# Optimization experiments

Measured on AMD Instinct MI355X. Metric: run time of the kernel, lower is better.

## Reference

```python
import jax, jax.numpy as jnp
import numpy as np

EPS = 1e-5
NEG_SLOPE = 0.2
GN_GROUPS = 8


def conv2d(x, w, b):
    # x: [B,C,H,W], w: [O,I,3,3]
    y = jax.lax.conv_general_dilated(
        x, w, window_strides=(1, 1), padding=((1, 1), (1, 1)),
        dimension_numbers=('NCHW', 'OIHW', 'NCHW'))
    return y + b[None, :, None, None]


def conv3d_d(x, w, b):
    # x: [B,C,D,H,W], w: [O,I,3,1,1] -> conv along D only
    y = jax.lax.conv_general_dilated(
        x, w, window_strides=(1, 1, 1), padding=((1, 1), (0, 0), (0, 0)),
        dimension_numbers=('NCDHW', 'OIDHW', 'NCDHW'))
    return y + b[None, :, None, None, None]


def group_norm(x, gamma, beta):
    # x: [B,C,D,H,W]; normalize per group over (C/g, D, H, W)
    B, C, D, H, W = x.shape
    xg = x.reshape(B, GN_GROUPS, C // GN_GROUPS, D, H, W)
    mu = jnp.mean(xg, axis=(2, 3, 4, 5), keepdims=True)
    var = jnp.var(xg, axis=(2, 3, 4, 5), keepdims=True)
    xn = ((xg - mu) * jax.lax.rsqrt(var + EPS)).reshape(B, C, D, H, W)
    return xn * gamma[None, :, None, None, None] + beta[None, :, None, None, None]


def setup_inputs() -> dict:
    key = jax.random.key(0)
    ks = jax.random.split(key, 8)
    C = 32
    B, D, H, W = 2, 24, 160, 160
    s = lambda fan: 1.0 / np.sqrt(fan)
    return {
        'x': jax.random.normal(ks[0], (B, C, D, H, W), jnp.float32),
        'w_f1': jax.random.normal(ks[1], (2 * C, C, 3, 1, 1), jnp.float32) * s(C * 3),
        'b_f1': jnp.zeros((2 * C,), jnp.float32),
        'gn_g': jnp.ones((2 * C,), jnp.float32),
        'gn_b': jnp.zeros((2 * C,), jnp.float32),
        'w_f2': jax.random.normal(ks[2], (C, 2 * C, 3, 1, 1), jnp.float32) * s(2 * C * 3),
        'b_f2': jnp.zeros((C,), jnp.float32),
        'w_u': jax.random.normal(ks[3], (C, 2 * C, 3, 3), jnp.float32) * s(2 * C * 9),
        'b_u': jnp.zeros((C,), jnp.float32),
        'w_r': jax.random.normal(ks[4], (C, 2 * C, 3, 3), jnp.float32) * s(2 * C * 9),
        'b_r': jnp.zeros((C,), jnp.float32),
        'w_o': jax.random.normal(ks[5], (C, 2 * C, 3, 3), jnp.float32) * s(2 * C * 9),
        'b_o': jnp.zeros((C,), jnp.float32),
    }


def reference(x, w_f1, b_f1, gn_g, gn_b, w_f2, b_f2, w_u, b_u, w_r, b_r, w_o, b_o):
    B, C, D, H, W = x.shape

    # slice_flow: Conv3d(C->2C,(3,1,1)) -> GroupNorm(8) -> LeakyReLU(0.2) -> Conv3d(2C->C,(3,1,1))
    sf = conv3d_d(x, w_f1, b_f1)
    sf = group_norm(sf, gn_g, gn_b)
    sf = jnp.where(sf >= 0, sf, NEG_SLOPE * sf)
    slice_features = conv3d_d(sf, w_f2, b_f2)

    def gru_step(h, xd):
        combined = jnp.concatenate([xd, h], axis=1)
        update = jax.nn.sigmoid(conv2d(combined, w_u, b_u))
        reset = jax.nn.sigmoid(conv2d(combined, w_r, b_r))
        combined_reset = jnp.concatenate([xd, reset * h], axis=1)
        cand = jnp.tanh(conv2d(combined_reset, w_o, b_o))
        h_new = (1.0 - update) * h + update * cand
        return h_new, h_new

    xd = jnp.moveaxis(x, 2, 0)  # [D,B,C,H,W]
    h0 = jnp.zeros((B, C, H, W), x.dtype)
    _, fwd = jax.lax.scan(gru_step, h0, xd)                 # [D,B,C,H,W]
    _, bwd = jax.lax.scan(gru_step, h0, xd, reverse=True)   # aligned with xd order

    enhanced = xd + fwd + bwd                                # [D,B,C,H,W]
    return jnp.moveaxis(enhanced, 0, 2) + slice_features
```

## Files before the change

### kernel.cpp

```cpp
#include <hip/hip_runtime.h>
#include <hip/hip_bf16.h>
#include <stdint.h>

#define EPS_GN 1e-5f
#define NEG_SLOPE 0.2f

static constexpr int  Bn   = 2;
static constexpr int  Cn   = 32;
static constexpr int  Dn   = 24;
static constexpr int  Hn   = 160;
static constexpr int  Wn   = 160;
static constexpr int  HWn  = Hn * Wn;
static constexpr long DHWn = (long)Dn * HWn;
static constexpr long NPIX = (long)Bn * Dn * HWn;

using frag8  = __attribute__((ext_vector_type(8)))  short;
using accf16 = __attribute__((ext_vector_type(16))) float;

__device__ __forceinline__ float bf2f(__hip_bfloat16 v) { return __bfloat162float(v); }
__device__ __forceinline__ __hip_bfloat16 f2bf(float v) { return __float2bfloat16(v); }
__device__ __forceinline__ float sigm(float v) { return 1.f / (1.f + __expf(-v)); }
__device__ __forceinline__ float tanh_(float v) {
    float e = __expf(2.f * v);
    return 1.f - 2.f / (e + 1.f);
}

__global__ __launch_bounds__(256) void bpack1_kernel(
    const float* __restrict__ w, __hip_bfloat16* __restrict__ dst)
{
    int t = blockIdx.x * 256 + threadIdx.x;
    if (t >= 6 * 2 * 64 * 8) return;
    int j    = t & 7;
    int lane = (t >> 3) & 63;
    int idx  = t >> 9;
    int nt   = idx & 1;
    int kb   = idx >> 1;
    int o    = nt * 32 + (lane & 31);
    int k    = kb * 16 + (lane >> 5) * 8 + j;
    int ci   = k & 31;
    int kd   = k >> 5;
    dst[t] = f2bf(w[(o * 32 + ci) * 3 + kd]);
}

__global__ __launch_bounds__(256) void bpack2_kernel(
    const float* __restrict__ w, __hip_bfloat16* __restrict__ dst)
{
    int t = blockIdx.x * 256 + threadIdx.x;
    if (t >= 12 * 64 * 8) return;
    int j    = t & 7;
    int lane = (t >> 3) & 63;
    int kb   = t >> 9;
    int o    = lane & 31;
    int k    = kb * 16 + (lane >> 5) * 8 + j;
    int ci   = k & 63;
    int kd   = k >> 6;
    dst[t] = f2bf(w[(o * 64 + ci) * 3 + kd]);
}

__global__ __launch_bounds__(256) void bpack_kernel(
    const float* __restrict__ w, __hip_bfloat16* __restrict__ dst)
{
    int t = blockIdx.x * 256 + threadIdx.x;
    if (t >= 9 * 4 * 64 * 8) return;
    int j    = t & 7;
    int lane = (t >> 3) & 63;
    int kb   = (t >> 9) & 3;
    int tap  = t >> 11;
    int ci   = kb * 16 + (lane >> 5) * 8 + j;
    int o    = lane & 31;
    dst[t] = f2bf(w[(o * 64 + ci) * 9 + tap]);
}

__global__ __launch_bounds__(256) void tohwc_kernel(
    const float* __restrict__ x, __hip_bfloat16* __restrict__ xhwc)
{
    __shared__ float tile[32][65];
    int bd = blockIdx.y;
    int b  = bd / Dn, d = bd % Dn;
    int p0 = blockIdx.x * 64;
    const float* xb = x + (long)b * Cn * DHWn + (long)d * HWn + p0;
    for (int e = threadIdx.x; e < 2048; e += 256) {
        int c = e >> 6, p = e & 63;
        tile[c][p] = xb[(long)c * DHWn + p];
    }
    __syncthreads();
    __hip_bfloat16* ob = xhwc + ((long)bd * HWn + p0) * 32;
    for (int e = threadIdx.x; e < 2048; e += 256) {
        int p = e >> 5, c = e & 31;
        ob[p * 32 + c] = f2bf(tile[c][p]);
    }
}

__global__ __launch_bounds__(256) void conv1_mfma(
    const __hip_bfloat16* __restrict__ xhwc,
    const __hip_bfloat16* __restrict__ Bp1,
    const float* __restrict__ b1,
    int b,
    __hip_bfloat16* __restrict__ A,
    float* __restrict__ gsum, float* __restrict__ gsq)
{
    int wave = threadIdx.x >> 6;
    int lane = threadIdx.x & 63;
    int ml   = lane & 31;
    int kh   = lane >> 5;
    int tile0 = blockIdx.x * 8 + wave * 2;

    frag8 bf[6][2];
#pragma unroll
    for (int kb = 0; kb < 6; kb++)
#pragma unroll
        for (int nt = 0; nt < 2; nt++)
            bf[kb][nt] = *(const frag8*)(Bp1 + ((kb * 2 + nt) * 64 + lane) * 8);

    int d  = tile0 / 800;
    int p0 = (tile0 % 800) * 32;

    accf16 acc[2][2];
#pragma unroll
    for (int t = 0; t < 2; t++)
#pragma unroll
        for (int nt = 0; nt < 2; nt++)
#pragma unroll
            for (int i = 0; i < 16; i++) acc[t][nt][i] = 0.f;

    for (int kd = 0; kd < 3; kd++) {
        int dd = d + kd - 1;
        bool valid = (unsigned)dd < (unsigned)Dn;
        const __hip_bfloat16* rp = xhwc + ((long)(b * Dn + dd) * HWn) * 32;
#pragma unroll
        for (int h2 = 0; h2 < 2; h2++) {
            int kb = kd * 2 + h2;
#pragma unroll
            for (int t = 0; t < 2; t++) {
                frag8 a = {};
                if (valid)
                    a = *(const frag8*)(rp + (long)(p0 + t * 32 + ml) * 32 + h2 * 16 + kh * 8);
                acc[t][0] = __builtin_amdgcn_mfma_f32_32x32x16_bf16(a, bf[kb][0], acc[t][0], 0, 0, 0);
                acc[t][1] = __builtin_amdgcn_mfma_f32_32x32x16_bf16(a, bf[kb][1], acc[t][1], 0, 0, 0);
            }
        }
    }

    float bias[2] = { b1[ml], b1[32 + ml] };
    float s[2] = {0.f, 0.f}, q[2] = {0.f, 0.f};
    __hip_bfloat16* Ap = A + (long)d * HWn * 64;
#pragma unroll
    for (int t = 0; t < 2; t++) {
        int pb = p0 + t * 32;
#pragma unroll
        for (int nt = 0; nt < 2; nt++) {
#pragma unroll
            for (int i = 0; i < 16; i++) {
                int row = (i & 3) + 8 * (i >> 2) + 4 * kh;
                float v = acc[t][nt][i] + bias[nt];
                Ap[(long)(pb + row) * 64 + nt * 32 + ml] = f2bf(v);
                s[nt] += v;
                q[nt] += v * v;
            }
        }
    }
#pragma unroll
    for (int nt = 0; nt < 2; nt++) {
        s[nt] += __shfl_xor(s[nt], 32);
        q[nt] += __shfl_xor(q[nt], 32);
    }
    __shared__ float ss[64], sq[64];
    if (threadIdx.x < 64) { ss[threadIdx.x] = 0.f; sq[threadIdx.x] = 0.f; }
    __syncthreads();
    if (lane < 32) {
        atomicAdd(&ss[ml],      s[0]); atomicAdd(&sq[ml],      q[0]);
        atomicAdd(&ss[32 + ml], s[1]); atomicAdd(&sq[32 + ml], q[1]);
    }
    __syncthreads();
    if (threadIdx.x < 64) {
        atomicAdd(&gsum[b * 64 + threadIdx.x], ss[threadIdx.x]);
        atomicAdd(&gsq [b * 64 + threadIdx.x], sq[threadIdx.x]);
    }
}

__global__ __launch_bounds__(64) void finalize_kernel(
    const float* __restrict__ gsum, const float* __restrict__ gsq,
    const float* __restrict__ gn_g, const float* __restrict__ gn_b,
    float* __restrict__ scal, float* __restrict__ shft, int b)
{
    int ci = threadIdx.x;
    if (ci >= 64) return;
    int g = ci >> 3;
    float s = 0.f, qq = 0.f;
#pragma unroll
    for (int k = 0; k < 8; k++) {
        s  += gsum[b * 64 + g * 8 + k];
        qq += gsq [b * 64 + g * 8 + k];
    }
    float N   = 8.0f * (float)DHWn;
    float mu  = s / N;
    float var = qq / N - mu * mu;
    float rs  = rsqrtf(var + EPS_GN);
    float scv = rs * gn_g[ci];
    scal[b * 64 + ci] = scv;
    shft[b * 64 + ci] = gn_b[ci] - mu * scv;
}

__global__ __launch_bounds__(256) void act_kernel(
    __hip_bfloat16* __restrict__ A,
    const float* __restrict__ scal, const float* __restrict__ shft, int b)
{
    __shared__ float sc[64], sh[64];
    if (threadIdx.x < 64) {
        sc[threadIdx.x] = scal[b * 64 + threadIdx.x];
        sh[threadIdx.x] = shft[b * 64 + threadIdx.x];
    }
    __syncthreads();
    long i0 = ((long)blockIdx.x * 256 + threadIdx.x) * 8;
    __hip_bfloat16 loc[8];
    *(frag8*)loc = *(const frag8*)(A + i0);
    int c0 = (int)(i0 & 63);
#pragma unroll
    for (int j = 0; j < 8; j++) {
        float f  = bf2f(loc[j]);
        float an = fmaf(f, sc[c0 + j], sh[c0 + j]);
        loc[j]   = f2bf(fmaxf(an, NEG_SLOPE * an));
    }
    *(frag8*)(A + i0) = *(frag8*)loc;
}

__global__ __launch_bounds__(256) void conv2_mfma(
    const __hip_bfloat16* __restrict__ Aact,
    const __hip_bfloat16* __restrict__ Bp2,
    const float* __restrict__ b2,
    const float* __restrict__ x,
    float* __restrict__ out,
    int b)
{
    int wave = threadIdx.x >> 6;
    int lane = threadIdx.x & 63;
    int ml   = lane & 31;
    int kh   = lane >> 5;
    int tile0 = blockIdx.x * 8 + wave * 2;

    frag8 bf[12];
#pragma unroll
    for (int kb = 0; kb < 12; kb++)
        bf[kb] = *(const frag8*)(Bp2 + (kb * 64 + lane) * 8);

    int d  = tile0 / 800;
    int p0 = (tile0 % 800) * 32;

    accf16 acc[2];
#pragma unroll
    for (int t = 0; t < 2; t++)
#pragma unroll
        for (int i = 0; i < 16; i++) acc[t][i] = 0.f;

    for (int kd = 0; kd < 3; kd++) {
        int dd = d + kd - 1;
        bool valid = (unsigned)dd < (unsigned)Dn;
        const __hip_bfloat16* rp = Aact + (long)dd * HWn * 64;
#pragma unroll
        for (int qq = 0; qq < 4; qq++) {
            int kb = kd * 4 + qq;
#pragma unroll
            for (int t = 0; t < 2; t++) {
                frag8 a = {};
                if (valid)
                    a = *(const frag8*)(rp + (long)(p0 + t * 32 + ml) * 64 + qq * 16 + kh * 8);
                acc[t] = __builtin_amdgcn_mfma_f32_32x32x16_bf16(a, bf[kb], acc[t], 0, 0, 0);
            }
        }
    }

    __shared__ float tb[4][32][33];
    float bias = b2[ml];
    const float* xb = x   + (long)b * Cn * DHWn + (long)d * HWn;
    float*       ob = out + (long)b * Cn * DHWn + (long)d * HWn;
#pragma unroll
    for (int t = 0; t < 2; t++) {
        int pb = p0 + t * 32;
#pragma unroll
        for (int i = 0; i < 16; i++) {
            int row = (i & 3) + 8 * (i >> 2) + 4 * kh;
            tb[wave][row][ml] = acc[t][i] + bias;
        }
#pragma unroll
        for (int r2 = 0; r2 < 16; r2++) {
            int c = r2 * 2 + kh;
            float v = tb[wave][ml][c] + xb[(long)c * DHWn + pb + ml];
            ob[(long)c * DHWn + pb + ml] = v;
        }
    }
}

__global__ __launch_bounds__(256) void gru_gates_mfma(
    const __hip_bfloat16* __restrict__ xhwc,
    int dfwd, int dbwd,
    const __hip_bfloat16* __restrict__ hbf,
    const __hip_bfloat16* __restrict__ Bu,
    const __hip_bfloat16* __restrict__ Br,
    const float* __restrict__ bu, const float* __restrict__ br,
    float* __restrict__ ufrag,
    __hip_bfloat16* __restrict__ rhbf)
{
    int db   = blockIdx.y;
    int dir  = db >> 1, b = db & 1;
    int d    = dir ? dbwd : dfwd;
    int wave = threadIdx.x >> 6;
    int lane = threadIdx.x & 63;
    int ml   = lane & 31;
    int kh   = lane >> 5;

    const __hip_bfloat16* xb = xhwc + ((long)b * Dn + d) * HWn * 32;
    const __hip_bfloat16* hb = hbf  + (long)db * HWn * 32;

    int tile0 = blockIdx.x * 8 + wave * 2;
    int tb[2]   = { tile0 * 32, tile0 * 32 + 32 };
    int py0[2]  = { tb[0] / Wn, tb[1] / Wn };
    int px0[2]  = { tb[0] % Wn, tb[1] % Wn };

    accf16 au[2], ar[2];
#pragma unroll
    for (int t = 0; t < 2; t++)
#pragma unroll
        for (int i = 0; i < 16; i++) { au[t][i] = 0.f; ar[t][i] = 0.f; }

    for (int tap = 0; tap < 9; tap++) {
        int dy = tap / 3 - 1, dx = tap % 3 - 1;
        long poff[2]; bool ok[2];
#pragma unroll
        for (int t = 0; t < 2; t++) {
            int yy = py0[t] + dy;
            int xx = px0[t] + ml + dx;
            ok[t]   = ((unsigned)yy < (unsigned)Hn) & ((unsigned)xx < (unsigned)Wn);
            poff[t] = ((long)(yy * Wn + xx)) * 32;
        }
#pragma unroll
        for (int kb = 0; kb < 4; kb++) {
            frag8 bu_f = *(const frag8*)(Bu + ((tap * 4 + kb) * 64 + lane) * 8);
            frag8 br_f = *(const frag8*)(Br + ((tap * 4 + kb) * 64 + lane) * 8);
            int ch = kb * 16 + kh * 8;
            const __hip_bfloat16* bsel = (kb < 2) ? (xb + ch) : (hb + (ch - 32));
#pragma unroll
            for (int t = 0; t < 2; t++) {
                frag8 a = {};
                if (ok[t]) a = *(const frag8*)(bsel + poff[t]);
                au[t] = __builtin_amdgcn_mfma_f32_32x32x16_bf16(a, bu_f, au[t], 0, 0, 0);
                ar[t] = __builtin_amdgcn_mfma_f32_32x32x16_bf16(a, br_f, ar[t], 0, 0, 0);
            }
        }
    }

    int ch = ml;
    float bias_u = bu[ch], bias_r = br[ch];
#pragma unroll
    for (int t = 0; t < 2; t++) {
        int pb = tb[t];
        float* uf = ufrag + ((long)db * 800 + tile0 + t) * 1024 + lane * 16;
        __hip_bfloat16* rhb = rhbf + (long)db * HWn * 32;
#pragma unroll
        for (int i = 0; i < 16; i++) {
            int row = (i & 3) + 8 * (i >> 2) + 4 * kh;
            int pix = pb + row;
            float hp = bf2f(hb[(long)pix * 32 + ch]);
            float uu = sigm(au[t][i] + bias_u);
            float rr = sigm(ar[t][i] + bias_r);
            uf[i] = uu;
            rhb[(long)pix * 32 + ch] = f2bf(rr * hp);
        }
    }
}

__global__ __launch_bounds__(256) void gru_cand_mfma(
    const __hip_bfloat16* __restrict__ xhwc,
    int dfwd, int dbwd,
    const __hip_bfloat16* __restrict__ rhbf,
    const __hip_bfloat16* __restrict__ Bo,
    const float* __restrict__ bo,
    const float* __restrict__ ufrag,
    __hip_bfloat16* __restrict__ hbf,
    float* __restrict__ out)
{
    int db   = blockIdx.y;
    int dir  = db >> 1, b = db & 1;
    int d    = dir ? dbwd : dfwd;
    int wave = threadIdx.x >> 6;
    int lane = threadIdx.x & 63;
    int ml   = lane & 31;
    int kh   = lane >> 5;

    const __hip_bfloat16* xb  = xhwc + ((long)b * Dn + d) * HWn * 32;
    const __hip_bfloat16* rhb = rhbf + (long)db * HWn * 32;
    __hip_bfloat16*       hb  = hbf  + (long)db * HWn * 32;

    int tile0 = blockIdx.x * 8 + wave * 2;
    int tb[2]   = { tile0 * 32, tile0 * 32 + 32 };
    int py0[2]  = { tb[0] / Wn, tb[1] / Wn };
    int px0[2]  = { tb[0] % Wn, tb[1] % Wn };

    accf16 ao[2];
#pragma unroll
    for (int t = 0; t < 2; t++)
#pragma unroll
        for (int i = 0; i < 16; i++) ao[t][i] = 0.f;

    for (int tap = 0; tap < 9; tap++) {
        int dy = tap / 3 - 1, dx = tap % 3 - 1;
        long poff[2]; bool ok[2];
#pragma unroll
        for (int t = 0; t < 2; t++) {
            int yy = py0[t] + dy;
            int xx = px0[t] + ml + dx;
            ok[t]   = ((unsigned)yy < (unsigned)Hn) & ((unsigned)xx < (unsigned)Wn);
            poff[t] = ((long)(yy * Wn + xx)) * 32;
        }
#pragma unroll
        for (int kb = 0; kb < 4; kb++) {
            frag8 bo_f = *(const frag8*)(Bo + ((tap * 4 + kb) * 64 + lane) * 8);
            int ch = kb * 16 + kh * 8;
            const __hip_bfloat16* bsel = (kb < 2) ? (xb + ch) : (rhb + (ch - 32));
#pragma unroll
            for (int t = 0; t < 2; t++) {
                frag8 a = {};
                if (ok[t]) a = *(const frag8*)(bsel + poff[t]);
                ao[t] = __builtin_amdgcn_mfma_f32_32x32x16_bf16(a, bo_f, ao[t], 0, 0, 0);
            }
        }
    }

    int ch = ml;
    float bias_o = bo[ch];
#pragma unroll
    for (int t = 0; t < 2; t++) {
        int pb = tb[t];
        const float* uf = ufrag + ((long)db * 800 + tile0 + t) * 1024 + lane * 16;
        float* ob = out + ((long)b * Cn + ch) * DHWn + (long)d * HWn;
#pragma unroll
        for (int i = 0; i < 16; i++) {
            int row = (i & 3) + 8 * (i >> 2) + 4 * kh;
            int pix = pb + row;
            float c  = tanh_(ao[t][i] + bias_o);
            float uu = uf[i];
            float hp = bf2f(hb[(long)pix * 32 + ch]);
            float hn = (1.f - uu) * hp + uu * c;
            hb[(long)pix * 32 + ch] = f2bf(hn);
            ob[pix] += hn;
        }
    }
}

extern "C" void kernel_launch(void* const* d_in, const int* in_sizes, int n_in,
                              void* d_out, int out_size, void* d_ws, size_t ws_size,
                              hipStream_t stream)
{
    const float* x    = (const float*)d_in[0];
    const float* w_f1 = (const float*)d_in[1];
    const float* b_f1 = (const float*)d_in[2];
    const float* gn_g = (const float*)d_in[3];
    const float* gn_b = (const float*)d_in[4];
    const float* w_f2 = (const float*)d_in[5];
    const float* b_f2 = (const float*)d_in[6];
    const float* w_u  = (const float*)d_in[7];
    const float* b_u  = (const float*)d_in[8];
    const float* w_r  = (const float*)d_in[9];
    const float* b_r  = (const float*)d_in[10];
    const float* w_o  = (const float*)d_in[11];
    const float* b_o  = (const float*)d_in[12];
    float* out = (float*)d_out;

    char* ws = (char*)d_ws;
    __hip_bfloat16* Bp1 = (__hip_bfloat16*)ws;
    __hip_bfloat16* Bp2 = Bp1 + 6144;
    __hip_bfloat16* Bu  = Bp2 + 6144;
    __hip_bfloat16* Br  = Bu + 18432;
    __hip_bfloat16* Bo  = Br + 18432;
    float* gsum = (float*)(Bo + 18432);
    float* gsq  = gsum + 128;
    float* scal = gsq + 128;
    float* shft = scal + 128;
    char* big = (char*)(shft + 128);
    big = (char*)(((uintptr_t)big + 255) & ~(uintptr_t)255);

    __hip_bfloat16* xhwc = (__hip_bfloat16*)big;
    __hip_bfloat16* Apre = (__hip_bfloat16*)(big + 78643200L);
    __hip_bfloat16* hbf  = (__hip_bfloat16*)(big + 78643200L);
    __hip_bfloat16* rhbf = (__hip_bfloat16*)(big + 85196800L);
    float*          ufrag= (float*)        (big + 91750400L);

    size_t need = (size_t)(big - ws) + 157286400UL;
    if (ws_size < need) return;

    bpack1_kernel<<<24, 256, 0, stream>>>(w_f1, Bp1);
    bpack2_kernel<<<24, 256, 0, stream>>>(w_f2, Bp2);
    bpack_kernel<<<72, 256, 0, stream>>>(w_u, Bu);
    bpack_kernel<<<72, 256, 0, stream>>>(w_r, Br);
    bpack_kernel<<<72, 256, 0, stream>>>(w_o, Bo);
    hipMemsetAsync(gsum, 0, 256 * sizeof(float), stream);

    tohwc_kernel<<<dim3(400, Bn * Dn), 256, 0, stream>>>(x, xhwc);

    for (int b = 0; b < Bn; b++) {
        conv1_mfma<<<2400, 256, 0, stream>>>(xhwc, Bp1, b_f1, b, Apre, gsum, gsq);
        finalize_kernel<<<1, 64, 0, stream>>>(gsum, gsq, gn_g, gn_b, scal, shft, b);
        act_kernel<<<19200, 256, 0, stream>>>(Apre, scal, shft, b);
        conv2_mfma<<<2400, 256, 0, stream>>>(Apre, Bp2, b_f2, x, out, b);
    }

    hipMemsetAsync(hbf, 0, 6553600, stream);
    for (int s = 0; s < Dn; s++) {
        int dfwd = s, dbwd = Dn - 1 - s;
        gru_gates_mfma<<<dim3(100, 4), 256, 0, stream>>>(
            xhwc, dfwd, dbwd, hbf, Bu, Br, b_u, b_r, ufrag, rhbf);
        gru_cand_mfma<<<dim3(100, 4), 256, 0, stream>>>(
            xhwc, dfwd, dbwd, rhbf, Bo, b_o, ufrag, hbf, out);
    }
}
```

Before: 2.153 ms.

## Move update gate into candidate kernel, halve tiles per wave, ping-pong hidden state

The update-gate conv moves from the gates kernel into the candidate kernel, which now computes it alongside the candidate conv from the old hidden state. This removes the fp32 ufrag round-trip through global memory. Each wave now handles one 32-pixel tile instead of two, doubling the grid for the GRU kernels and conv2 to put more blocks on the CUs. The hidden state is double-buffered so the candidate kernel can read the old h while writing the new one. Output accumulation is transposed through shared memory for coalesced stores. In exchange, each B fragment is reused across fewer tiles and the candidate kernel does more work per step.

```diff
diff --git a/kernel.cpp b/kernel.cpp
--- a/kernel.cpp
+++ b/kernel.cpp
@@ -236,21 +236,19 @@
     int lane = threadIdx.x & 63;
     int ml   = lane & 31;
     int kh   = lane >> 5;
-    int tile0 = blockIdx.x * 8 + wave * 2;
+    int tile = blockIdx.x * 4 + wave;
 
     frag8 bf[12];
 #pragma unroll
     for (int kb = 0; kb < 12; kb++)
         bf[kb] = *(const frag8*)(Bp2 + (kb * 64 + lane) * 8);
 
-    int d  = tile0 / 800;
-    int p0 = (tile0 % 800) * 32;
-
-    accf16 acc[2];
-#pragma unroll
-    for (int t = 0; t < 2; t++)
-#pragma unroll
-        for (int i = 0; i < 16; i++) acc[t][i] = 0.f;
+    int d  = tile / 800;
+    int p0 = (tile % 800) * 32;
+
+    accf16 acc;
+#pragma unroll
+    for (int i = 0; i < 16; i++) acc[i] = 0.f;
 
     for (int kd = 0; kd < 3; kd++) {
         int dd = d + kd - 1;
@@ -258,14 +256,10 @@
         const __hip_bfloat16* rp = Aact + (long)dd * HWn * 64;
 #pragma unroll
         for (int qq = 0; qq < 4; qq++) {
-            int kb = kd * 4 + qq;
-#pragma unroll
-            for (int t = 0; t < 2; t++) {
-                frag8 a = {};
-                if (valid)
-                    a = *(const frag8*)(rp + (long)(p0 + t * 32 + ml) * 64 + qq * 16 + kh * 8);
-                acc[t] = __builtin_amdgcn_mfma_f32_32x32x16_bf16(a, bf[kb], acc[t], 0, 0, 0);
-            }
+            frag8 a = {};
+            if (valid)
+                a = *(const frag8*)(rp + (long)(p0 + ml) * 64 + qq * 16 + kh * 8);
+            acc = __builtin_amdgcn_mfma_f32_32x32x16_bf16(a, bf[kd * 4 + qq], acc, 0, 0, 0);
         }
     }
 
@@ -274,30 +268,24 @@
     const float* xb = x   + (long)b * Cn * DHWn + (long)d * HWn;
     float*       ob = out + (long)b * Cn * DHWn + (long)d * HWn;
 #pragma unroll
-    for (int t = 0; t < 2; t++) {
-        int pb = p0 + t * 32;
-#pragma unroll
-        for (int i = 0; i < 16; i++) {
-            int row = (i & 3) + 8 * (i >> 2) + 4 * kh;
-            tb[wave][row][ml] = acc[t][i] + bias;
-        }
-#pragma unroll
-        for (int r2 = 0; r2 < 16; r2++) {
-            int c = r2 * 2 + kh;
-            float v = tb[wave][ml][c] + xb[(long)c * DHWn + pb + ml];
-            ob[(long)c * DHWn + pb + ml] = v;
-        }
-    }
-}
-
-__global__ __launch_bounds__(256) void gru_gates_mfma(
+    for (int i = 0; i < 16; i++) {
+        int row = (i & 3) + 8 * (i >> 2) + 4 * kh;
+        tb[wave][row][ml] = acc[i] + bias;
+    }
+#pragma unroll
+    for (int r2 = 0; r2 < 16; r2++) {
+        int c = r2 * 2 + kh;
+        float v = tb[wave][ml][c] + xb[(long)c * DHWn + p0 + ml];
+        ob[(long)c * DHWn + p0 + ml] = v;
+    }
+}
+
+__global__ __launch_bounds__(256) void gru_r_mfma(
     const __hip_bfloat16* __restrict__ xhwc,
     int dfwd, int dbwd,
-    const __hip_bfloat16* __restrict__ hbf,
-    const __hip_bfloat16* __restrict__ Bu,
+    const __hip_bfloat16* __restrict__ hold,
     const __hip_bfloat16* __restrict__ Br,
-    const float* __restrict__ bu, const float* __restrict__ br,
-    float* __restrict__ ufrag,
+    const float* __restrict__ br,
     __hip_bfloat16* __restrict__ rhbf)
 {
     int db   = blockIdx.y;
@@ -309,73 +297,54 @@
     int kh   = lane >> 5;
 
     const __hip_bfloat16* xb = xhwc + ((long)b * Dn + d) * HWn * 32;
-    const __hip_bfloat16* hb = hbf  + (long)db * HWn * 32;
-
-    int tile0 = blockIdx.x * 8 + wave * 2;
-    int tb[2]   = { tile0 * 32, tile0 * 32 + 32 };
-    int py0[2]  = { tb[0] / Wn, tb[1] / Wn };
-    int px0[2]  = { tb[0] % Wn, tb[1] % Wn };
-
-    accf16 au[2], ar[2];
-#pragma unroll
-    for (int t = 0; t < 2; t++)
-#pragma unroll
-        for (int i = 0; i < 16; i++) { au[t][i] = 0.f; ar[t][i] = 0.f; }
+    const __hip_bfloat16* hb = hold + (long)db * HWn * 32;
+
+    int tile = blockIdx.x * 4 + wave;
+    int pb   = tile * 32;
+    int py0  = pb / Wn, px0 = pb % Wn;
+
+    accf16 ar;
+#pragma unroll
+    for (int i = 0; i < 16; i++) ar[i] = 0.f;
 
     for (int tap = 0; tap < 9; tap++) {
         int dy = tap / 3 - 1, dx = tap % 3 - 1;
-        long poff[2]; bool ok[2];
-#pragma unroll
-        for (int t = 0; t < 2; t++) {
-            int yy = py0[t] + dy;
-            int xx = px0[t] + ml + dx;
-            ok[t]   = ((unsigned)yy < (unsigned)Hn) & ((unsigned)xx < (unsigned)Wn);
-            poff[t] = ((long)(yy * Wn + xx)) * 32;
-        }
+        int yy = py0 + dy;
+        int xx = px0 + ml + dx;
+        bool ok  = ((unsigned)yy < (unsigned)Hn) & ((unsigned)xx < (unsigned)Wn);
+        long poff = ((long)(yy * Wn + xx)) * 32;
 #pragma unroll
         for (int kb = 0; kb < 4; kb++) {
-            frag8 bu_f = *(const frag8*)(Bu + ((tap * 4 + kb) * 64 + lane) * 8);
-            frag8 br_f = *(const frag8*)(Br + ((tap * 4 + kb) * 64 + lane) * 8);
+            frag8 brf = *(const frag8*)(Br + ((tap * 4 + kb) * 64 + lane) * 8);
             int ch = kb * 16 + kh * 8;
             const __hip_bfloat16* bsel = (kb < 2) ? (xb + ch) : (hb + (ch - 32));
-#pragma unroll
-            for (int t = 0; t < 2; t++) {
-                frag8 a = {};
-                if (ok[t]) a = *(const frag8*)(bsel + poff[t]);
-                au[t] = __builtin_amdgcn_mfma_f32_32x32x16_bf16(a, bu_f, au[t], 0, 0, 0);
-                ar[t] = __builtin_amdgcn_mfma_f32_32x32x16_bf16(a, br_f, ar[t], 0, 0, 0);
-            }
+            frag8 a = {};
+            if (ok) a = *(const frag8*)(bsel + poff);
+            ar = __builtin_amdgcn_mfma_f32_32x32x16_bf16(a, brf, ar, 0, 0, 0);
         }
     }
 
-    int ch = ml;
-    float bias_u = bu[ch], bias_r = br[ch];
-#pragma unroll
-    for (int t = 0; t < 2; t++) {
-        int pb = tb[t];
-        float* uf = ufrag + ((long)db * 800 + tile0 + t) * 1024 + lane * 16;
-        __hip_bfloat16* rhb = rhbf + (long)db * HWn * 32;
-#pragma unroll
-        for (int i = 0; i < 16; i++) {
-            int row = (i & 3) + 8 * (i >> 2) + 4 * kh;
-            int pix = pb + row;
-            float hp = bf2f(hb[(long)pix * 32 + ch]);
-            float uu = sigm(au[t][i] + bias_u);
-            float rr = sigm(ar[t][i] + bias_r);
-            uf[i] = uu;
-            rhb[(long)pix * 32 + ch] = f2bf(rr * hp);
-        }
+    float bias_r = br[ml];
+    __hip_bfloat16* rhb = rhbf + (long)db * HWn * 32;
+#pragma unroll
+    for (int i = 0; i < 16; i++) {
+        int row = (i & 3) + 8 * (i >> 2) + 4 * kh;
+        int pix = pb + row;
+        float hp = bf2f(hb[(long)pix * 32 + ml]);
+        float rr = sigm(ar[i] + bias_r);
+        rhb[(long)pix * 32 + ml] = f2bf(rr * hp);
     }
 }
 
 __global__ __launch_bounds__(256) void gru_cand_mfma(
     const __hip_bfloat16* __restrict__ xhwc,
     int dfwd, int dbwd,
+    const __hip_bfloat16* __restrict__ hold,
     const __hip_bfloat16* __restrict__ rhbf,
+    const __hip_bfloat16* __restrict__ Bu,
     const __hip_bfloat16* __restrict__ Bo,
-    const float* __restrict__ bo,
-    const float* __restrict__ ufrag,
-    __hip_bfloat16* __restrict__ hbf,
+    const float* __restrict__ bu, const float* __restrict__ bo,
+    __hip_bfloat16* __restrict__ hnew,
     float* __restrict__ out)
 {
     int db   = blockIdx.y;
@@ -387,62 +356,64 @@
     int kh   = lane >> 5;
 
     const __hip_bfloat16* xb  = xhwc + ((long)b * Dn + d) * HWn * 32;
+    const __hip_bfloat16* hb  = hold + (long)db * HWn * 32;
     const __hip_bfloat16* rhb = rhbf + (long)db * HWn * 32;
-    __hip_bfloat16*       hb  = hbf  + (long)db * HWn * 32;
-
-    int tile0 = blockIdx.x * 8 + wave * 2;
-    int tb[2]   = { tile0 * 32, tile0 * 32 + 32 };
-    int py0[2]  = { tb[0] / Wn, tb[1] / Wn };
-    int px0[2]  = { tb[0] % Wn, tb[1] % Wn };
-
-    accf16 ao[2];
-#pragma unroll
-    for (int t = 0; t < 2; t++)
-#pragma unroll
-        for (int i = 0; i < 16; i++) ao[t][i] = 0.f;
+    __hip_bfloat16*       hnb = hnew + (long)db * HWn * 32;
+
+    int tile = blockIdx.x * 4 + wave;
+    int pb   = tile * 32;
+    int py0  = pb / Wn, px0 = pb % Wn;
+
+    accf16 au, ao;
+#pragma unroll
+    for (int i = 0; i < 16; i++) { au[i] = 0.f; ao[i] = 0.f; }
 
     for (int tap = 0; tap < 9; tap++) {
         int dy = tap / 3 - 1, dx = tap % 3 - 1;
-        long poff[2]; bool ok[2];
-#pragma unroll
-        for (int t = 0; t < 2; t++) {
-            int yy = py0[t] + dy;
-            int xx = px0[t] + ml + dx;
-            ok[t]   = ((unsigned)yy < (unsigned)Hn) & ((unsigned)xx < (unsigned)Wn);
-            poff[t] = ((long)(yy * Wn + xx)) * 32;
-        }
+        int yy = py0 + dy;
+        int xx = px0 + ml + dx;
+        bool ok  = ((unsigned)yy < (unsigned)Hn) & ((unsigned)xx < (unsigned)Wn);
+        long poff = ((long)(yy * Wn + xx)) * 32;
 #pragma unroll
         for (int kb = 0; kb < 4; kb++) {
-            frag8 bo_f = *(const frag8*)(Bo + ((tap * 4 + kb) * 64 + lane) * 8);
+            frag8 buf = *(const frag8*)(Bu + ((tap * 4 + kb) * 64 + lane) * 8);
+            frag8 bof = *(const frag8*)(Bo + ((tap * 4 + kb) * 64 + lane) * 8);
             int ch = kb * 16 + kh * 8;
-            const __hip_bfloat16* bsel = (kb < 2) ? (xb + ch) : (rhb + (ch - 32));
-#pragma unroll
-            for (int t = 0; t < 2; t++) {
+            if (kb < 2) {
                 frag8 a = {};
-                if (ok[t]) a = *(const frag8*)(bsel + poff[t]);
-                ao[t] = __builtin_amdgcn_mfma_f32_32x32x16_bf16(a, bo_f, ao[t], 0, 0, 0);
+                if (ok) a = *(const frag8*)(xb + ch + poff);
+                au = __builtin_amdgcn_mfma_f32_32x32x16_bf16(a, buf, au, 0, 0, 0);
+                ao = __builtin_amdgcn_mfma_f32_32x32x16_bf16(a, bof, ao, 0, 0, 0);
+            } else {
+                frag8 ah = {}, arh = {};
+                if (ok) {
+                    ah  = *(const frag8*)(hb  + (ch - 32) + poff);
+                    arh = *(const frag8*)(rhb + (ch - 32) + poff);
+                }
+                au = __builtin_amdgcn_mfma_f32_32x32x16_bf16(ah,  buf, au, 0, 0, 0);
+                ao = __builtin_amdgcn_mfma_f32_32x32x16_bf16(arh, bof, ao, 0, 0, 0);
             }
         }
     }
 
-    int ch = ml;
-    float bias_o = bo[ch];
-#pragma unroll
-    for (int t = 0; t < 2; t++) {
-        int pb = tb[t];
-        const float* uf = ufrag + ((long)db * 800 + tile0 + t) * 1024 + lane * 16;
-        float* ob = out + ((long)b * Cn + ch) * DHWn + (long)d * HWn;
-#pragma unroll
-        for (int i = 0; i < 16; i++) {
-            int row = (i & 3) + 8 * (i >> 2) + 4 * kh;
-            int pix = pb + row;
-            float c  = tanh_(ao[t][i] + bias_o);
-            float uu = uf[i];
-            float hp = bf2f(hb[(long)pix * 32 + ch]);
-            float hn = (1.f - uu) * hp + uu * c;
-            hb[(long)pix * 32 + ch] = f2bf(hn);
-            ob[pix] += hn;
-        }
+    __shared__ float tb[4][32][33];
+    float bias_u = bu[ml], bias_o = bo[ml];
+    float* ob = out + (long)b * Cn * DHWn + (long)d * HWn;
+#pragma unroll
+    for (int i = 0; i < 16; i++) {
+        int row = (i & 3) + 8 * (i >> 2) + 4 * kh;
+        int pix = pb + row;
+        float uu = sigm(au[i] + bias_u);
+        float cc = tanh_(ao[i] + bias_o);
+        float hp = bf2f(hb[(long)pix * 32 + ml]);
+        float hn = (1.f - uu) * hp + uu * cc;
+        hnb[(long)pix * 32 + ml] = f2bf(hn);
+        tb[wave][row][ml] = hn;
+    }
+#pragma unroll
+    for (int r2 = 0; r2 < 16; r2++) {
+        int c = r2 * 2 + kh;
+        ob[(long)c * DHWn + pb + ml] += tb[wave][ml][c];
     }
 }
 
@@ -480,9 +451,9 @@
 
     __hip_bfloat16* xhwc = (__hip_bfloat16*)big;
     __hip_bfloat16* Apre = (__hip_bfloat16*)(big + 78643200L);
-    __hip_bfloat16* hbf  = (__hip_bfloat16*)(big + 78643200L);
-    __hip_bfloat16* rhbf = (__hip_bfloat16*)(big + 85196800L);
-    float*          ufrag= (float*)        (big + 91750400L);
+    __hip_bfloat16* hA   = (__hip_bfloat16*)(big + 78643200L);
+    __hip_bfloat16* hB   = (__hip_bfloat16*)(big + 85196800L);
+    __hip_bfloat16* rhbf = (__hip_bfloat16*)(big + 91750400L);
 
     size_t need = (size_t)(big - ws) + 157286400UL;
     if (ws_size < need) return;
@@ -500,15 +471,18 @@
         conv1_mfma<<<2400, 256, 0, stream>>>(xhwc, Bp1, b_f1, b, Apre, gsum, gsq);
         finalize_kernel<<<1, 64, 0, stream>>>(gsum, gsq, gn_g, gn_b, scal, shft, b);
         act_kernel<<<19200, 256, 0, stream>>>(Apre, scal, shft, b);
-        conv2_mfma<<<2400, 256, 0, stream>>>(Apre, Bp2, b_f2, x, out, b);
-    }
-
-    hipMemsetAsync(hbf, 0, 6553600, stream);
+        conv2_mfma<<<4800, 256, 0, stream>>>(Apre, Bp2, b_f2, x, out, b);
+    }
+
+    hipMemsetAsync(hA, 0, 6553600, stream);
+    __hip_bfloat16* hbufs[2] = { hA, hB };
     for (int s = 0; s < Dn; s++) {
         int dfwd = s, dbwd = Dn - 1 - s;
-        gru_gates_mfma<<<dim3(100, 4), 256, 0, stream>>>(
-            xhwc, dfwd, dbwd, hbf, Bu, Br, b_u, b_r, ufrag, rhbf);
-        gru_cand_mfma<<<dim3(100, 4), 256, 0, stream>>>(
-            xhwc, dfwd, dbwd, rhbf, Bo, b_o, ufrag, hbf, out);
-    }
-}
+        __hip_bfloat16* hold = hbufs[s & 1];
+        __hip_bfloat16* hnew = hbufs[(s + 1) & 1];
+        gru_r_mfma<<<dim3(200, 4), 256, 0, stream>>>(
+            xhwc, dfwd, dbwd, hold, Br, b_r, rhbf);
+        gru_cand_mfma<<<dim3(200, 4), 256, 0, stream>>>(
+            xhwc, dfwd, dbwd, hold, rhbf, Bu, Bo, b_u, b_o, hnew, out);
+    }
+}
```

Result: faster. 1.996 ms (-7.3%).
